# Kernel tuning notes

Hardware: AMD Instinct MI355X
Metric: run time of the kernel (lower is better)

## Reference

```python
import jax, jax.numpy as jnp
import numpy as np

L, H, DK = 4, 8, 64
NEG = -1e9
PAD = -9999.0


def _ln(z, g, b, eps=1e-6):
    # LayerNormalization: uses unbiased std (torch default) and divides by (std + eps)
    m = jnp.mean(z, axis=-1, keepdims=True)
    s = jnp.std(z, axis=-1, keepdims=True, ddof=1)
    return g * (z - m) / (s + eps) + b


def _mha(q_in, kv_in, w, bw, pw, pb, lnp, mask):
    B, Sq, D = q_in.shape
    q = (q_in @ w[0] + bw[0]).reshape(B, Sq, H, DK).transpose(0, 2, 1, 3)
    k = (kv_in @ w[1] + bw[1]).reshape(B, -1, H, DK).transpose(0, 2, 1, 3)
    v = (kv_in @ w[2] + bw[2]).reshape(B, -1, H, DK).transpose(0, 2, 1, 3)
    scores = jnp.einsum('bhqd,bhkd->bhqk', q, k) * (1.0 / np.sqrt(DK))
    if mask is not None:
        scores = jnp.where(mask[:, None, :, :], NEG, scores)
    attn = jax.nn.softmax(scores, axis=-1)
    ctx = jnp.einsum('bhqk,bhkd->bhqd', attn, v).transpose(0, 2, 1, 3).reshape(B, Sq, H * DK)
    return _ln(q_in + ctx @ pw + pb, lnp[0], lnp[1])


def _ffn(x, w1, b1, w2, b2, lnp):
    # kernel-1 conv1d == pointwise linear; w1:[d_ff,d_model], w2:[d_model,d_ff]
    h = jax.nn.relu(jnp.einsum('bsd,fd->bsf', x, w1) + b1)
    o = jnp.einsum('bsf,df->bsd', h, w2) + b2
    return _ln(x + o, lnp[0], lnp[1])


def _forward(enc_inputs, dec_inputs, emb_w, emb_b, pos_table,
             e_qkv_w, e_qkv_b, e_pw, e_pb, e_ln1, e_w1, e_b1, e_w2, e_b2, e_ln2,
             ds_qkv_w, ds_qkv_b, ds_pw, ds_pb, d_ln1,
             dc_qkv_w, dc_qkv_b, dc_pw, dc_pb, d_ln2,
             d_w1, d_b1, d_w2, d_b2, d_ln3):
    B, Se, F = enc_inputs.shape
    Sd = dec_inputs.shape[1]
    # ConvEmbeddingLayer: kernel-1 conv producing (d_model - n_features) channels, concat with raw inputs
    enc = jnp.concatenate([enc_inputs, jnp.einsum('bsf,of->bso', enc_inputs, emb_w) + emb_b], axis=-1)
    dec = jnp.concatenate([dec_inputs, jnp.einsum('bsf,of->bso', dec_inputs, emb_w) + emb_b], axis=-1)
    # PosEncoding with full lengths -> rows 1..S of the padded table
    enc = enc + pos_table[1:Se + 1]
    dec = dec + pos_table[1:Sd + 1]
    # masks per get_attn_pad_mask / get_attn_subsequent_mask
    enc_pad = jnp.sum(enc_inputs, axis=-1) <= PAD  # [B,Se]
    dec_pad = jnp.sum(dec_inputs, axis=-1) <= PAD  # [B,Sd]
    enc_mask = jnp.broadcast_to(enc_pad[:, None, :], (B, Se, Se))
    causal = jnp.triu(jnp.ones((Sd, Sd), dtype=bool), 1)
    dec_self_mask = jnp.broadcast_to(dec_pad[:, None, :], (B, Sd, Sd)) | causal
    cross_mask = jnp.broadcast_to(enc_pad[:, None, :], (B, Sd, Se))
    for i in range(L):
        enc = _mha(enc, enc, e_qkv_w[i], e_qkv_b[i], e_pw[i], e_pb[i], e_ln1[i], enc_mask)
        enc = _ffn(enc, e_w1[i], e_b1[i], e_w2[i], e_b2[i], e_ln2[i])
    for i in range(L):
        dec = _mha(dec, dec, ds_qkv_w[i], ds_qkv_b[i], ds_pw[i], ds_pb[i], d_ln1[i], dec_self_mask)
        dec = _mha(dec, enc, dc_qkv_w[i], dc_qkv_b[i], dc_pw[i], dc_pb[i], d_ln2[i], cross_mask)
        dec = _ffn(dec, d_w1[i], d_b1[i], d_w2[i], d_b2[i], d_ln3[i])
    return dec


def setup_inputs() -> dict:
    B, Se, Sd, F, Dm, Dff = 8, 512, 512, 32, 512, 2048
    key = jax.random.key(0)
    ks = iter(jax.random.split(key, 32))
    s = 0.02

    def n(shape, sc=s):
        return jax.random.normal(next(ks), shape, jnp.float32) * sc

    # sinusoidal PosEncoding table with leading pad row
    pos = np.arange(Se, dtype=np.float64)[:, None]
    j = np.arange(Dm)[None, :]
    ang = pos / np.power(10000.0, 2.0 * (j // 2) / Dm)
    ang[:, 0::2] = np.sin(ang[:, 0::2])
    ang[:, 1::2] = np.cos(ang[:, 1::2])
    pos_table = jnp.asarray(np.concatenate([np.zeros((1, Dm)), ang]).astype(np.float32))

    ln = jnp.broadcast_to(jnp.stack([jnp.ones(Dm), jnp.zeros(Dm)]), (L, 2, Dm)).astype(jnp.float32) + 0.0
    return {
        'enc_inputs': jax.random.normal(next(ks), (B, Se, F), jnp.float32),
        'dec_inputs': jax.random.normal(next(ks), (B, Sd, F), jnp.float32),
        'emb_w': n((Dm - F, F)), 'emb_b': jnp.zeros(Dm - F, jnp.float32),
        'pos_table': pos_table,
        'e_qkv_w': n((L, 3, Dm, H * DK)), 'e_qkv_b': jnp.zeros((L, 3, H * DK), jnp.float32),
        'e_pw': n((L, H * DK, Dm)), 'e_pb': jnp.zeros((L, Dm), jnp.float32), 'e_ln1': ln,
        'e_w1': n((L, Dff, Dm)), 'e_b1': jnp.zeros((L, Dff), jnp.float32),
        'e_w2': n((L, Dm, Dff)), 'e_b2': jnp.zeros((L, Dm), jnp.float32), 'e_ln2': ln,
        'ds_qkv_w': n((L, 3, Dm, H * DK)), 'ds_qkv_b': jnp.zeros((L, 3, H * DK), jnp.float32),
        'ds_pw': n((L, H * DK, Dm)), 'ds_pb': jnp.zeros((L, Dm), jnp.float32), 'd_ln1': ln,
        'dc_qkv_w': n((L, 3, Dm, H * DK)), 'dc_qkv_b': jnp.zeros((L, 3, H * DK), jnp.float32),
        'dc_pw': n((L, H * DK, Dm)), 'dc_pb': jnp.zeros((L, Dm), jnp.float32), 'd_ln2': ln,
        'd_w1': n((L, Dff, Dm)), 'd_b1': jnp.zeros((L, Dff), jnp.float32),
        'd_w2': n((L, Dm, Dff)), 'd_b2': jnp.zeros((L, Dm), jnp.float32), 'd_ln3': ln,
    }


def reference(enc_inputs, dec_inputs, emb_w, emb_b, pos_table,
              e_qkv_w, e_qkv_b, e_pw, e_pb, e_ln1, e_w1, e_b1, e_w2, e_b2, e_ln2,
              ds_qkv_w, ds_qkv_b, ds_pw, ds_pb, d_ln1,
              dc_qkv_w, dc_qkv_b, dc_pw, dc_pb, d_ln2,
              d_w1, d_b1, d_w2, d_b2, d_ln3):
    return _forward(enc_inputs, dec_inputs, emb_w, emb_b, pos_table,
                    e_qkv_w, e_qkv_b, e_pw, e_pb, e_ln1, e_w1, e_b1, e_w2, e_b2, e_ln2,
                    ds_qkv_w, ds_qkv_b, ds_pw, ds_pb, d_ln1,
                    dc_qkv_w, dc_qkv_b, dc_pw, dc_pb, d_ln2,
                    d_w1, d_b1, d_w2, d_b2, d_ln3)
```

## Files before the change

kernel.cpp:

```cpp
#include <hip/hip_runtime.h>
#include <cstdint>
#include <cstddef>

typedef unsigned short u16;
typedef __bf16 bf16x8 __attribute__((ext_vector_type(8)));
typedef float f32x4 __attribute__((ext_vector_type(4)));

constexpr int Bz = 8, Sq = 512, Hh = 8, DKd = 64, Dm = 512, Dff = 2048, NL = 4;
constexpr int TOK = Bz * Sq;
constexpr size_t MAT = (size_t)512 * 512;
constexpr size_t EL  = (size_t)TOK * Dm;
constexpr size_t WFT = (size_t)Dff * Dm;

__device__ __forceinline__ float bf2f(u16 u) {
  union { uint32_t i; float f; } v; v.i = (uint32_t)u << 16; return v.f;
}
__device__ __forceinline__ u16 f2bf(float f) {
  union { float f; uint32_t i; } v; v.f = f;
  uint32_t i = v.i;
  i += 0x7fffu + ((i >> 16) & 1u);
  return (u16)(i >> 16);
}

__device__ __forceinline__ void gload16(const u16* g, u16* l) {
  __builtin_amdgcn_global_load_lds(
      (const __attribute__((address_space(1))) unsigned int*)g,
      (__attribute__((address_space(3))) unsigned int*)l, 16, 0, 0);
}

template<int BM, int BN, int TAG>
__global__ __launch_bounds__(256)
void gemm_tile(const u16* __restrict__ A, const u16* __restrict__ Bt,
               const float* __restrict__ bias, u16* __restrict__ C,
               int K, int lda, long long sA, int ldb, long long sB,
               int ldc, long long sC, int cmode, int relu, int colofs,
               const u16* A2, int xsplit, const float* __restrict__ posp)
{
  constexpr int HM = BM / 2, HN = BN / 2, MI = HM / 16, NI = HN / 16;
  constexpr int LV = BM / 32 + BN / 32;
  static_assert(LV == 4 || LV == 6 || LV == 8, "unsupported tile");
  __shared__ __align__(16) u16 As[2][BM * 64];
  __shared__ __align__(16) u16 Bs[2][BN * 64];
  const int bz = blockIdx.z;
  const u16* Abase = A;
  int colbase;
  if (A2 && (int)blockIdx.x >= xsplit) {
    Abase = A2;
    colbase = 512 + ((int)blockIdx.x - xsplit) * BN;
  } else {
    colbase = colofs + (int)blockIdx.x * BN;
  }
  const u16* Ab = Abase + (size_t)bz * (size_t)sA + (size_t)(blockIdx.y * BM) * lda;
  const u16* Bb = Bt + (size_t)bz * (size_t)sB + (size_t)colbase * ldb;
  const int tid  = threadIdx.x;
  const int lane = tid & 63;
  const int l15  = lane & 15;
  const int quad = lane >> 4;
  const int wid  = tid >> 6;
  const int wm   = wid >> 1, wn = wid & 1;

  f32x4 acc[MI][NI] = {};

  auto STAGE = [&](int buf, int k0) {
#pragma unroll
    for (int i = 0; i < BM / 32; ++i) {
      const int s = tid + i * 256;
      const int row = s >> 3, c = (s & 7) ^ (row & 7);
      gload16(Ab + (size_t)row * lda + k0 + c * 8, &As[buf][s * 8]);
    }
#pragma unroll
    for (int i = 0; i < BN / 32; ++i) {
      const int s = tid + i * 256;
      const int row = s >> 3, c = (s & 7) ^ (row & 7);
      gload16(Bb + (size_t)row * ldb + k0 + c * 8, &Bs[buf][s * 8]);
    }
  };

  auto COMPUTE = [&](int buf) {
#pragma unroll
    for (int kk = 0; kk < 2; ++kk) {
      bf16x8 af[MI], bfr[NI];
#pragma unroll
      for (int mi = 0; mi < MI; ++mi) {
        const int ra = wm * HM + mi * 16 + l15;
        af[mi] = *(const bf16x8*)(&As[buf][ra * 64 + (((kk * 4 + quad) ^ (ra & 7))) * 8]);
      }
#pragma unroll
      for (int ni = 0; ni < NI; ++ni) {
        const int rb = wn * HN + ni * 16 + l15;
        bfr[ni] = *(const bf16x8*)(&Bs[buf][rb * 64 + (((kk * 4 + quad) ^ (rb & 7))) * 8]);
      }
#pragma unroll
      for (int mi = 0; mi < MI; ++mi)
#pragma unroll
        for (int ni = 0; ni < NI; ++ni)
          acc[mi][ni] = __builtin_amdgcn_mfma_f32_16x16x32_bf16(af[mi], bfr[ni], acc[mi][ni], 0, 0, 0);
    }
  };

  STAGE(0, 0);
  const int NT = K >> 6;
  int cur = 0;
  for (int t = 0; t < NT - 1; ++t) {
    STAGE(cur ^ 1, (t + 1) << 6);
    if constexpr (LV == 4)      asm volatile("s_waitcnt vmcnt(4)" ::: "memory");
    else if constexpr (LV == 6) asm volatile("s_waitcnt vmcnt(6)" ::: "memory");
    else                        asm volatile("s_waitcnt vmcnt(8)" ::: "memory");
    __builtin_amdgcn_s_barrier();
    COMPUTE(cur);
    asm volatile("s_waitcnt lgkmcnt(0)" ::: "memory");
    __builtin_amdgcn_s_barrier();
    cur ^= 1;
  }
  asm volatile("s_waitcnt vmcnt(0)" ::: "memory");
  __builtin_amdgcn_s_barrier();
  COMPUTE(cur);

  const int rblk = blockIdx.y * BM + wm * HM + quad * 4;
#pragma unroll
  for (int ni = 0; ni < NI; ++ni) {
    const int colx = colbase + wn * HN + ni * 16 + l15;
    const float bv = bias ? bias[colx] : 0.f;
#pragma unroll
    for (int mi = 0; mi < MI; ++mi) {
#pragma unroll
      for (int r = 0; r < 4; ++r) {
        float v = acc[mi][ni][r] + bv;
        if (relu) v = fmaxf(v, 0.f);
        const int grow = rblk + mi * 16 + r;
        size_t off;
        if (cmode == 0) {
          off = (size_t)bz * (size_t)sC + (size_t)grow * ldc + colx;
        } else if (cmode == 5) {
          const int s = grow & 511;
          v += posp[(size_t)(s + 1) * 512 + colx];
          off = (size_t)grow * 512 + colx;
        } else {
          const int sec = colx >> 9, n = colx & 511, h = n >> 6, d = n & 63;
          const int b = grow >> 9, s = grow & 511;
          if (sec == 0) v *= 0.125f;
          if (sec < 2) off = (size_t)sec * EL + (size_t)b * 262144 + (size_t)h * 32768 + (size_t)s * 64 + d;
          else         off = 2 * EL + (size_t)b * 262144 + (size_t)h * 32768 + (size_t)d * 512 + s;
        }
        C[off] = f2bf(v);
      }
    }
  }
}

__global__ __launch_bounds__(256)
void flash_attn(const u16* __restrict__ q, const u16* __restrict__ k,
                const u16* __restrict__ v, const unsigned char* __restrict__ pad,
                u16* __restrict__ ctx, int mtype)
{
  __shared__ __align__(16) u16 KVs[8192];
  __shared__ __align__(16) u16 Pw[4][2048];
  const int bh = blockIdx.y, b = bh >> 3, h = bh & 7;
  const int qt = blockIdx.x;
  const int tid = threadIdx.x, lane = tid & 63, wid = tid >> 6;
  const int l15 = lane & 15, quad = lane >> 4;
  const size_t bho = (size_t)bh * 32768;
  const int qrow = qt * 64 + wid * 16 + l15;
  const int qcd  = qt * 64 + wid * 16 + quad * 4;

  unsigned char* Ps = (unsigned char*)&Pw[0][0];
  if (tid < 128) ((uchar4*)Ps)[tid] = ((const uchar4*)(pad + b * 512))[tid];

  bf16x8 aq0 = *(const bf16x8*)(q + bho + (size_t)qrow * 64 + quad * 8);
  bf16x8 aq1 = *(const bf16x8*)(q + bho + (size_t)qrow * 64 + 32 + quad * 8);

  f32x4 S[32];
#pragma unroll
  for (int kc = 0; kc < 4; ++kc) {
    __syncthreads();
#pragma unroll
    for (int i = 0; i < 4; ++i) {
      const int s = tid + i * 256;
      const int row = s >> 3, c = (s & 7) ^ (row & 7);
      gload16(k + bho + (size_t)(kc * 128 + row) * 64 + c * 8, KVs + s * 8);
    }
    __syncthreads();
#pragma unroll
    for (int t = 0; t < 8; ++t) {
      const int sw = l15 & 7;
      bf16x8 b0 = *(const bf16x8*)(KVs + (t * 16 + l15) * 64 + (quad ^ sw) * 8);
      bf16x8 b1 = *(const bf16x8*)(KVs + (t * 16 + l15) * 64 + ((4 + quad) ^ sw) * 8);
      f32x4 z = {0.f, 0.f, 0.f, 0.f};
      z = __builtin_amdgcn_mfma_f32_16x16x32_bf16(aq0, b0, z, 0, 0, 0);
      S[kc * 8 + t] = __builtin_amdgcn_mfma_f32_16x16x32_bf16(aq1, b1, z, 0, 0, 0);
    }
  }

  unsigned pm = 0u;
#pragma unroll
  for (int t = 0; t < 32; ++t) pm |= (unsigned)(Ps[t * 16 + l15] != 0) << t;

  float inv[4];
#pragma unroll
  for (int r = 0; r < 4; ++r) {
    const int qg = qcd + r;
    float mx = -3.0e38f;
#pragma unroll
    for (int t = 0; t < 32; ++t) {
      const int col = t * 16 + l15;
      const bool m = ((pm >> t) & 1u) || (mtype == 1 && col > qg);
      const float val = m ? -1e9f : S[t][r];
      S[t][r] = val;
      mx = fmaxf(mx, val);
    }
#pragma unroll
    for (int o = 8; o > 0; o >>= 1) mx = fmaxf(mx, __shfl_xor(mx, o));
    float sm = 0.f;
#pragma unroll
    for (int t = 0; t < 32; ++t) { const float e = __expf(S[t][r] - mx); S[t][r] = e; sm += e; }
#pragma unroll
    for (int o = 8; o > 0; o >>= 1) sm += __shfl_xor(sm, o);
    inv[r] = 1.f / sm;
  }

  f32x4 O[4] = {};
  u16* myP = &Pw[wid][0];
#pragma unroll
  for (int kc = 0; kc < 4; ++kc) {
    __syncthreads();
#pragma unroll
    for (int i = 0; i < 4; ++i) {
      const int s = tid + i * 256;
      const int row = s >> 4, c = (s & 15) ^ (row & 15);
      gload16(v + bho + (size_t)row * 512 + kc * 128 + c * 8, KVs + s * 8);
    }
#pragma unroll
    for (int t = 0; t < 8; ++t)
#pragma unroll
      for (int r = 0; r < 4; ++r) {
        const int rowq = quad * 4 + r;
        const int c = 2 * t + (l15 >> 3);
        myP[rowq * 128 + (c ^ rowq) * 8 + (l15 & 7)] = f2bf(S[kc * 8 + t][r] * inv[r]);
      }
    __syncthreads();
#pragma unroll
    for (int kk = 0; kk < 4; ++kk) {
      bf16x8 ap = *(const bf16x8*)(myP + l15 * 128 + ((kk * 4 + quad) ^ l15) * 8);
#pragma unroll
      for (int ni = 0; ni < 4; ++ni) {
        bf16x8 bv = *(const bf16x8*)(KVs + (ni * 16 + l15) * 128 + ((kk * 4 + quad) ^ l15) * 8);
        O[ni] = __builtin_amdgcn_mfma_f32_16x16x32_bf16(ap, bv, O[ni], 0, 0, 0);
      }
    }
  }

  const int token = b * 512 + qcd;
#pragma unroll
  for (int ni = 0; ni < 4; ++ni)
#pragma unroll
    for (int r = 0; r < 4; ++r)
      ctx[(size_t)(token + r) * 512 + h * 64 + ni * 16 + l15] = f2bf(O[ni][r]);
}

__global__ __launch_bounds__(256)
void prep_weights(const float* __restrict__ s0, const float* __restrict__ s1,
                  const float* __restrict__ s2, const float* __restrict__ s3,
                  const float* __restrict__ s4, const float* __restrict__ s5,
                  u16* __restrict__ outT,
                  const float* __restrict__ c0, const float* __restrict__ c1,
                  const float* __restrict__ c2, const float* __restrict__ c3,
                  u16* __restrict__ outC,
                  const float* __restrict__ ew, const float* __restrict__ eb,
                  u16* __restrict__ ewb, float* __restrict__ biasE,
                  const float* __restrict__ xe, const float* __restrict__ xd,
                  u16* __restrict__ xbf,
                  unsigned char* __restrict__ pe, unsigned char* __restrict__ pd)
{
  __shared__ float tile[32][33];
  const int z = blockIdx.z;
  const int tid = threadIdx.y * 32 + threadIdx.x;
  const int r  = tid >> 3;
  const int c4 = (tid & 7) * 4;
  if (z < 48) {
    const float* src; int zi;
    if      (z < 12) { src = s0; zi = z; }
    else if (z < 24) { src = s1; zi = z - 12; }
    else if (z < 36) { src = s2; zi = z - 24; }
    else if (z < 40) { src = s3; zi = z - 36; }
    else if (z < 44) { src = s4; zi = z - 40; }
    else             { src = s5; zi = z - 44; }
    const float* in = src + (size_t)zi * MAT;
    u16* o = outT + (size_t)z * MAT;
    float4 v = *(const float4*)(in + (size_t)(blockIdx.y * 32 + r) * 512 + blockIdx.x * 32 + c4);
    tile[r][c4 + 0] = v.x; tile[r][c4 + 1] = v.y;
    tile[r][c4 + 2] = v.z; tile[r][c4 + 3] = v.w;
    __syncthreads();
    ushort4 w;
    w.x = f2bf(tile[c4 + 0][r]);
    w.y = f2bf(tile[c4 + 1][r]);
    w.z = f2bf(tile[c4 + 2][r]);
    w.w = f2bf(tile[c4 + 3][r]);
    *(ushort4*)(o + (size_t)(blockIdx.x * 32 + r) * 512 + blockIdx.y * 32 + c4) = w;
  } else if (z < 112) {
    const int L = (z - 48) * 256 + blockIdx.y * 16 + blockIdx.x;
    const int tens = L >> 12, bx = L & 4095;
    const float* srcs[4] = { c0, c1, c2, c3 };
    const float* src = srcs[tens];
    u16* dst = outC + (size_t)tens * (4 * WFT);
    const int i = (bx * 256 + tid) * 4;
    float4 v = *(const float4*)(src + i);
    ushort4 u = { f2bf(v.x), f2bf(v.y), f2bf(v.z), f2bf(v.w) };
    *(ushort4*)(dst + i) = u;
  } else if (z == 112) {
    const int bxy = blockIdx.y * 16 + blockIdx.x;
    if (tid < 128) {
      const int row = bxy * 2 + (tid >> 6);
      const int c = tid & 63;
      float v;
      if (row < 32) v = (c == row) ? 1.f : 0.f;
      else          v = (c < 32) ? ew[(size_t)(row - 32) * 32 + c] : 0.f;
      ewb[(size_t)row * 64 + c] = f2bf(v);
    }
    if (bxy == 0) {
#pragma unroll
      for (int rep = 0; rep < 2; ++rep) {
        const int i = tid + rep * 256;
        biasE[i] = (i < 32) ? 0.f : eb[i - 32];
      }
    }
  } else {
    const int bxy = blockIdx.y * 16 + blockIdx.x;
    const int lw = tid & 31;
#pragma unroll
    for (int rep = 0; rep < 4; ++rep) {
      const int rr0 = bxy * 32 + rep * 8 + (tid >> 5);
      const float* xsrc = (rr0 < 4096) ? xe : xd;
      const int rr = rr0 & 4095;
      const float v = xsrc[(size_t)rr * 32 + lw];
      float sm = v;
#pragma unroll
      for (int o = 16; o > 0; o >>= 1) sm += __shfl_xor(sm, o);
      if (lw == 0) {
        unsigned char* pv = (rr0 < 4096) ? pe : pd;
        pv[rr] = (sm <= -9999.f) ? 1 : 0;
      }
      u16* orow = xbf + (size_t)rr0 * 64;
      orow[lw] = f2bf(v);
      orow[32 + lw] = 0;
    }
  }
}

__global__ __launch_bounds__(256)
void add_ln(const u16* __restrict__ x, const u16* __restrict__ y,
            const float* __restrict__ g, const float* __restrict__ bb,
            u16* __restrict__ out, float* __restrict__ out32)
{
  const int row  = blockIdx.x * 4 + (threadIdx.x >> 6);
  const int lane = threadIdx.x & 63;
  const int c0 = lane * 8;
  const size_t base = (size_t)row * Dm + c0;

  uint4 xr = *(const uint4*)(x + base);
  uint4 yr = *(const uint4*)(y + base);
  const u16* xh = (const u16*)&xr;
  const u16* yh = (const u16*)&yr;
  float z[8];
  float s = 0.f;
#pragma unroll
  for (int j = 0; j < 8; ++j) { z[j] = bf2f(xh[j]) + bf2f(yh[j]); s += z[j]; }
#pragma unroll
  for (int off = 32; off > 0; off >>= 1) s += __shfl_xor(s, off);
  const float mean = s * (1.f / 512.f);
  float ss = 0.f;
#pragma unroll
  for (int j = 0; j < 8; ++j) { z[j] -= mean; ss += z[j] * z[j]; }
#pragma unroll
  for (int off = 32; off > 0; off >>= 1) ss += __shfl_xor(ss, off);
  const float stdv = sqrtf(ss * (1.f / 511.f));
  const float inv = 1.f / (stdv + 1e-6f);

  float4 g0 = *(const float4*)(g + c0),  g1 = *(const float4*)(g + c0 + 4);
  float4 b0 = *(const float4*)(bb + c0), b1 = *(const float4*)(bb + c0 + 4);
  float gv[8] = { g0.x, g0.y, g0.z, g0.w, g1.x, g1.y, g1.z, g1.w };
  float bv[8] = { b0.x, b0.y, b0.z, b0.w, b1.x, b1.y, b1.z, b1.w };
  float o[8];
#pragma unroll
  for (int j = 0; j < 8; ++j) o[j] = gv[j] * z[j] * inv + bv[j];
  if (out32) {
    float4 w0 = { o[0], o[1], o[2], o[3] };
    float4 w1 = { o[4], o[5], o[6], o[7] };
    *(float4*)(out32 + base) = w0;
    *(float4*)(out32 + base + 4) = w1;
  } else {
    uint4 ow;
    u16* oh = (u16*)&ow;
#pragma unroll
    for (int j = 0; j < 8; ++j) oh[j] = f2bf(o[j]);
    *(uint4*)(out + base) = ow;
  }
}

extern "C" void kernel_launch(void* const* d_in, const int* in_sizes, int n_in,
                              void* d_out, int out_size, void* d_ws, size_t ws_size,
                              hipStream_t stream)
{
  (void)in_sizes; (void)n_in; (void)out_size;
  const float* enc_in   = (const float*)d_in[0];
  const float* dec_in   = (const float*)d_in[1];
  const float* emb_w    = (const float*)d_in[2];
  const float* emb_b    = (const float*)d_in[3];
  const float* pos      = (const float*)d_in[4];
  const float* e_qkv_w  = (const float*)d_in[5];
  const float* e_qkv_b  = (const float*)d_in[6];
  const float* e_pw     = (const float*)d_in[7];
  const float* e_pb     = (const float*)d_in[8];
  const float* e_ln1    = (const float*)d_in[9];
  const float* e_w1     = (const float*)d_in[10];
  const float* e_b1     = (const float*)d_in[11];
  const float* e_w2     = (const float*)d_in[12];
  const float* e_b2     = (const float*)d_in[13];
  const float* e_ln2    = (const float*)d_in[14];
  const float* ds_qkv_w = (const float*)d_in[15];
  const float* ds_qkv_b = (const float*)d_in[16];
  const float* ds_pw    = (const float*)d_in[17];
  const float* ds_pb    = (const float*)d_in[18];
  const float* d_ln1    = (const float*)d_in[19];
  const float* dc_qkv_w = (const float*)d_in[20];
  const float* dc_qkv_b = (const float*)d_in[21];
  const float* dc_pw    = (const float*)d_in[22];
  const float* dc_pb    = (const float*)d_in[23];
  const float* d_ln2    = (const float*)d_in[24];
  const float* d_w1     = (const float*)d_in[25];
  const float* d_b1     = (const float*)d_in[26];
  const float* d_w2     = (const float*)d_in[27];
  const float* d_b2     = (const float*)d_in[28];
  const float* d_ln3    = (const float*)d_in[29];

  u16* ws  = (u16*)d_ws;
  u16* enc = ws;
  u16* dec = ws + EL;
  u16* qb  = ws + 2 * EL;
  u16* kb  = ws + 3 * EL;
  u16* vT  = ws + 4 * EL;
  u16* ctx = ws + 5 * EL;
  u16* t1  = ws + 6 * EL;
  u16* hff = ws + 7 * EL;
  u16* wT  = ws + 15 * EL;
  unsigned char* padE = (unsigned char*)(ws + 21 * EL);
  unsigned char* padD = padE + TOK;
  u16* xbf   = ws + 21 * EL + 8192;
  u16* ewb   = xbf + (size_t)8192 * 64;
  float* biasE = (float*)(ewb + 32768);
  u16* wfAll = ws + 22 * EL;
  if (ws_size < 30 * EL * 2 + 2 * TOK) return;

  prep_weights<<<dim3(16, 16, 114), dim3(32, 8), 0, stream>>>(
      e_qkv_w, ds_qkv_w, dc_qkv_w, e_pw, ds_pw, dc_pw, wT,
      e_w1, e_w2, d_w1, d_w2, wfAll,
      emb_w, emb_b, ewb, biasE,
      enc_in, dec_in, xbf, padE, padD);
  gemm_tile<64, 128, 4><<<dim3(4, 128, 1), 256, 0, stream>>>(
      xbf, ewb, biasE, enc, 64, 64, 0, 64, 0, 512, 0, 5, 0, 0, nullptr, 0, pos);

  auto attention = [&](const u16* qsrc, const u16* kvsrc, const u16* wq3, const float* b3,
                       const u16* pwT, const float* pb, const float* ln,
                       const unsigned char* pad, int mtype, u16* x) {
    if (qsrc == kvsrc) {
      gemm_tile<64, 128, 0><<<dim3(12, 64, 1), 256, 0, stream>>>(
          qsrc, wq3, b3, qb, 512, 512, 0, 512, 0, 0, 0, 4, 0, 0, nullptr, 0, nullptr);
    } else {
      gemm_tile<64, 128, 0><<<dim3(12, 64, 1), 256, 0, stream>>>(
          qsrc, wq3, b3, qb, 512, 512, 0, 512, 0, 0, 0, 4, 0, 0, kvsrc, 4, nullptr);
    }
    flash_attn<<<dim3(8, 64), 256, 0, stream>>>(qb, kb, vT, pad, ctx, mtype);
    gemm_tile<64, 64, 1><<<dim3(8, 64, 1), 256, 0, stream>>>(
        ctx, pwT, pb, t1, 512, 512, 0, 512, 0, 512, 0, 0, 0, 0, nullptr, 0, nullptr);
    add_ln<<<TOK / 4, 256, 0, stream>>>(x, t1, ln, ln + 512, x, nullptr);
  };

  auto ffn = [&](u16* x, const u16* w1b, const float* b1, const u16* w2b,
                 const float* b2, const float* ln, float* o32) {
    gemm_tile<64, 128, 2><<<dim3(16, 64, 1), 256, 0, stream>>>(
        x, w1b, b1, hff, 512, 512, 0, 512, 0, 2048, 0, 0, 1, 0, nullptr, 0, nullptr);
    gemm_tile<64, 64, 3><<<dim3(8, 64, 1), 256, 0, stream>>>(
        hff, w2b, b2, t1, 2048, 2048, 0, 2048, 0, 512, 0, 0, 0, 0, nullptr, 0, nullptr);
    add_ln<<<TOK / 4, 256, 0, stream>>>(x, t1, ln, ln + 512, x, o32);
  };

  for (int i = 0; i < NL; ++i) {
    attention(enc, enc, wT + (size_t)(i * 3) * MAT, e_qkv_b + i * 3 * 512,
              wT + (size_t)(36 + i) * MAT, e_pb + i * 512, e_ln1 + i * 1024, padE, 0, enc);
    ffn(enc, wfAll + (size_t)i * WFT, e_b1 + i * Dff,
        wfAll + 4 * WFT + (size_t)i * WFT, e_b2 + i * Dm, e_ln2 + i * 1024, nullptr);
  }

  for (int i = 0; i < NL; ++i) {
    attention(dec, dec, wT + (size_t)(12 + i * 3) * MAT, ds_qkv_b + i * 3 * 512,
              wT + (size_t)(40 + i) * MAT, ds_pb + i * 512, d_ln1 + i * 1024, padD, 1, dec);
    attention(dec, enc, wT + (size_t)(24 + i * 3) * MAT, dc_qkv_b + i * 3 * 512,
              wT + (size_t)(44 + i) * MAT, dc_pb + i * 512, d_ln2 + i * 1024, padE, 2, dec);
    ffn(dec, wfAll + 8 * WFT + (size_t)i * WFT, d_b1 + i * Dff,
        wfAll + 12 * WFT + (size_t)i * WFT, d_b2 + i * Dm, d_ln3 + i * 1024,
        (i == NL - 1) ? (float*)d_out : nullptr);
  }
}
```

Measured before the change: 1.294 ms.

## Single-buffer GEMM staging, coalesce V-transpose store via LDS, widen weight conversion

The GEMM drops its double-buffered LDS pipeline with manual waitcnt and uses a single buffer with __syncthreads around each K step. V-section outputs in the QKV GEMM are now transposed through LDS and written as 16-byte row stores instead of scattered 2-byte writes. The FFN weight fp32-to-bf16 conversion handles 8 elements per thread, so the prep grid shrinks. The V store change targets uncoalesced writes, but losing the load/compute overlap may expose global memory latency in every GEMM.

```diff
diff --git a/kernel.cpp b/kernel.cpp
--- a/kernel.cpp
+++ b/kernel.cpp
@@ -37,10 +37,8 @@
                const u16* A2, int xsplit, const float* __restrict__ posp)
 {
   constexpr int HM = BM / 2, HN = BN / 2, MI = HM / 16, NI = HN / 16;
-  constexpr int LV = BM / 32 + BN / 32;
-  static_assert(LV == 4 || LV == 6 || LV == 8, "unsupported tile");
-  __shared__ __align__(16) u16 As[2][BM * 64];
-  __shared__ __align__(16) u16 Bs[2][BN * 64];
+  __shared__ __align__(16) u16 As[BM * 64];
+  __shared__ __align__(16) u16 Bs[BN * 64];
   const int bz = blockIdx.z;
   const u16* Abase = A;
   int colbase;
@@ -54,41 +52,39 @@
   const u16* Bb = Bt + (size_t)bz * (size_t)sB + (size_t)colbase * ldb;
   const int tid  = threadIdx.x;
   const int lane = tid & 63;
+  const int wid  = tid >> 6;
   const int l15  = lane & 15;
   const int quad = lane >> 4;
-  const int wid  = tid >> 6;
   const int wm   = wid >> 1, wn = wid & 1;
 
   f32x4 acc[MI][NI] = {};
 
-  auto STAGE = [&](int buf, int k0) {
+  for (int k0 = 0; k0 < K; k0 += 64) {
 #pragma unroll
     for (int i = 0; i < BM / 32; ++i) {
       const int s = tid + i * 256;
       const int row = s >> 3, c = (s & 7) ^ (row & 7);
-      gload16(Ab + (size_t)row * lda + k0 + c * 8, &As[buf][s * 8]);
+      gload16(Ab + (size_t)row * lda + k0 + c * 8, As + s * 8);
     }
 #pragma unroll
     for (int i = 0; i < BN / 32; ++i) {
       const int s = tid + i * 256;
       const int row = s >> 3, c = (s & 7) ^ (row & 7);
-      gload16(Bb + (size_t)row * ldb + k0 + c * 8, &Bs[buf][s * 8]);
-    }
-  };
-
-  auto COMPUTE = [&](int buf) {
+      gload16(Bb + (size_t)row * ldb + k0 + c * 8, Bs + s * 8);
+    }
+    __syncthreads();
 #pragma unroll
     for (int kk = 0; kk < 2; ++kk) {
       bf16x8 af[MI], bfr[NI];
 #pragma unroll
       for (int mi = 0; mi < MI; ++mi) {
         const int ra = wm * HM + mi * 16 + l15;
-        af[mi] = *(const bf16x8*)(&As[buf][ra * 64 + (((kk * 4 + quad) ^ (ra & 7))) * 8]);
+        af[mi] = *(const bf16x8*)(As + ra * 64 + (((kk * 4 + quad) ^ (ra & 7))) * 8);
       }
 #pragma unroll
       for (int ni = 0; ni < NI; ++ni) {
         const int rb = wn * HN + ni * 16 + l15;
-        bfr[ni] = *(const bf16x8*)(&Bs[buf][rb * 64 + (((kk * 4 + quad) ^ (rb & 7))) * 8]);
+        bfr[ni] = *(const bf16x8*)(Bs + rb * 64 + (((kk * 4 + quad) ^ (rb & 7))) * 8);
       }
 #pragma unroll
       for (int mi = 0; mi < MI; ++mi)
@@ -96,54 +92,64 @@
         for (int ni = 0; ni < NI; ++ni)
           acc[mi][ni] = __builtin_amdgcn_mfma_f32_16x16x32_bf16(af[mi], bfr[ni], acc[mi][ni], 0, 0, 0);
     }
-  };
-
-  STAGE(0, 0);
-  const int NT = K >> 6;
-  int cur = 0;
-  for (int t = 0; t < NT - 1; ++t) {
-    STAGE(cur ^ 1, (t + 1) << 6);
-    if constexpr (LV == 4)      asm volatile("s_waitcnt vmcnt(4)" ::: "memory");
-    else if constexpr (LV == 6) asm volatile("s_waitcnt vmcnt(6)" ::: "memory");
-    else                        asm volatile("s_waitcnt vmcnt(8)" ::: "memory");
-    __builtin_amdgcn_s_barrier();
-    COMPUTE(cur);
-    asm volatile("s_waitcnt lgkmcnt(0)" ::: "memory");
-    __builtin_amdgcn_s_barrier();
-    cur ^= 1;
-  }
-  asm volatile("s_waitcnt vmcnt(0)" ::: "memory");
-  __builtin_amdgcn_s_barrier();
-  COMPUTE(cur);
+    __syncthreads();
+  }
 
   const int rblk = blockIdx.y * BM + wm * HM + quad * 4;
-#pragma unroll
-  for (int ni = 0; ni < NI; ++ni) {
-    const int colx = colbase + wn * HN + ni * 16 + l15;
-    const float bv = bias ? bias[colx] : 0.f;
-#pragma unroll
-    for (int mi = 0; mi < MI; ++mi) {
-#pragma unroll
-      for (int r = 0; r < 4; ++r) {
-        float v = acc[mi][ni][r] + bv;
-        if (relu) v = fmaxf(v, 0.f);
-        const int grow = rblk + mi * 16 + r;
-        size_t off;
-        if (cmode == 0) {
-          off = (size_t)bz * (size_t)sC + (size_t)grow * ldc + colx;
-        } else if (cmode == 5) {
-          const int s = grow & 511;
-          v += posp[(size_t)(s + 1) * 512 + colx];
-          off = (size_t)grow * 512 + colx;
-        } else {
-          const int sec = colx >> 9, n = colx & 511, h = n >> 6, d = n & 63;
-          const int b = grow >> 9, s = grow & 511;
-          if (sec == 0) v *= 0.125f;
-          if (sec < 2) off = (size_t)sec * EL + (size_t)b * 262144 + (size_t)h * 32768 + (size_t)s * 64 + d;
-          else         off = 2 * EL + (size_t)b * 262144 + (size_t)h * 32768 + (size_t)d * 512 + s;
+  if (cmode != 4 || colbase < 1024) {
+#pragma unroll
+    for (int ni = 0; ni < NI; ++ni) {
+      const int colx = colbase + wn * HN + ni * 16 + l15;
+      const float bv = bias ? bias[colx] : 0.f;
+#pragma unroll
+      for (int mi = 0; mi < MI; ++mi) {
+#pragma unroll
+        for (int r = 0; r < 4; ++r) {
+          float v = acc[mi][ni][r] + bv;
+          if (relu) v = fmaxf(v, 0.f);
+          const int grow = rblk + mi * 16 + r;
+          size_t off;
+          if (cmode == 0) {
+            off = (size_t)bz * (size_t)sC + (size_t)grow * ldc + colx;
+          } else if (cmode == 5) {
+            const int s = grow & 511;
+            v += posp[(size_t)(s + 1) * 512 + colx];
+            off = (size_t)grow * 512 + colx;
+          } else {
+            const int sec = colx >> 9, n = colx & 511, h = n >> 6, d = n & 63;
+            const int b = grow >> 9, s = grow & 511;
+            if (sec == 0) v *= 0.125f;
+            off = (size_t)sec * EL + (size_t)b * 262144 + (size_t)h * 32768 + (size_t)s * 64 + d;
+          }
+          C[off] = f2bf(v);
         }
-        C[off] = f2bf(v);
-      }
+      }
+    }
+  } else {
+    u16* Ls = Bs;
+#pragma unroll
+    for (int ni = 0; ni < NI; ++ni) {
+      const int col = wn * HN + ni * 16 + l15;
+      const float bv = bias ? bias[colbase + col] : 0.f;
+#pragma unroll
+      for (int mi = 0; mi < MI; ++mi) {
+#pragma unroll
+        for (int r = 0; r < 4; ++r) {
+          const int srow = wm * HM + mi * 16 + quad * 4 + r;
+          Ls[col * 64 + (srow ^ ((col & 7) << 3))] = f2bf(acc[mi][ni][r] + bv);
+        }
+      }
+    }
+    __syncthreads();
+    const int gb = (blockIdx.y * BM) >> 9, s0 = (blockIdx.y * BM) & 511;
+    const int grp = tid >> 3, sl = tid & 7;
+    u16* vdst = C + 2 * EL + (size_t)gb * 262144 + s0;
+#pragma unroll
+    for (int j = 0; j < BN / 32; ++j) {
+      const int col = j * 32 + grp;
+      const int n = (colbase - 1024) + col, h = n >> 6, d = n & 63;
+      uint4 w = *(const uint4*)(Ls + col * 64 + ((sl ^ (col & 7)) << 3));
+      *(uint4*)(vdst + (size_t)h * 32768 + (size_t)d * 512 + sl * 8) = w;
     }
   }
 }
@@ -296,17 +302,24 @@
     w.z = f2bf(tile[c4 + 2][r]);
     w.w = f2bf(tile[c4 + 3][r]);
     *(ushort4*)(o + (size_t)(blockIdx.x * 32 + r) * 512 + blockIdx.y * 32 + c4) = w;
-  } else if (z < 112) {
+  } else if (z < 80) {
     const int L = (z - 48) * 256 + blockIdx.y * 16 + blockIdx.x;
-    const int tens = L >> 12, bx = L & 4095;
+    const size_t e0 = ((size_t)L * 256 + tid) * 8;
+    const int tens = (int)(e0 >> 22);
+    const size_t local = e0 & (4 * WFT - 1);
     const float* srcs[4] = { c0, c1, c2, c3 };
     const float* src = srcs[tens];
-    u16* dst = outC + (size_t)tens * (4 * WFT);
-    const int i = (bx * 256 + tid) * 4;
-    float4 v = *(const float4*)(src + i);
-    ushort4 u = { f2bf(v.x), f2bf(v.y), f2bf(v.z), f2bf(v.w) };
-    *(ushort4*)(dst + i) = u;
-  } else if (z == 112) {
+    float4 v0 = *(const float4*)(src + local);
+    float4 v1 = *(const float4*)(src + local + 4);
+    ushort4 ua = { f2bf(v0.x), f2bf(v0.y), f2bf(v0.z), f2bf(v0.w) };
+    ushort4 ub = { f2bf(v1.x), f2bf(v1.y), f2bf(v1.z), f2bf(v1.w) };
+    uint4 w;
+    w.x = (uint32_t)ua.x | ((uint32_t)ua.y << 16);
+    w.y = (uint32_t)ua.z | ((uint32_t)ua.w << 16);
+    w.z = (uint32_t)ub.x | ((uint32_t)ub.y << 16);
+    w.w = (uint32_t)ub.z | ((uint32_t)ub.w << 16);
+    *(uint4*)(outC + (size_t)tens * (4 * WFT) + local) = w;
+  } else if (z == 80) {
     const int bxy = blockIdx.y * 16 + blockIdx.x;
     if (tid < 128) {
       const int row = bxy * 2 + (tid >> 6);
@@ -450,7 +463,7 @@
   u16* wfAll = ws + 22 * EL;
   if (ws_size < 30 * EL * 2 + 2 * TOK) return;
 
-  prep_weights<<<dim3(16, 16, 114), dim3(32, 8), 0, stream>>>(
+  prep_weights<<<dim3(16, 16, 82), dim3(32, 8), 0, stream>>>(
       e_qkv_w, ds_qkv_w, dc_qkv_w, e_pw, ds_pw, dc_pw, wT,
       e_w1, e_w2, d_w1, d_w2, wfAll,
       emb_w, emb_b, ewb, biasE,
```

After: 1.255 ms. 1.03x faster.
